# Kernel optimization log

Hardware: AMD Instinct MI355X
Metric: run time of the kernel (lower is better)

The kernel has to match this reference:

```python
import jax, jax.numpy as jnp
import numpy as np

NUM_MOVIES = 100000
MOVIE_FEAT = 128
USER_FEAT = 128
BATCH = 16384
N_NBRS = 50
D0, D1, D2 = 256, 256, 128  # layer_dims


def setup_inputs() -> dict:
    key = jax.random.key(0)
    ks = jax.random.split(key, 16)
    inp = {
        "users": jax.random.normal(ks[0], (BATCH, USER_FEAT), jnp.float32),
        "pos_movies": jax.random.normal(ks[1], (BATCH, MOVIE_FEAT), jnp.float32),
        "neg_movies": jax.random.normal(ks[2], (BATCH, MOVIE_FEAT), jnp.float32),
        "user_ids": jax.random.randint(ks[3], (BATCH,), 0, BATCH),
        "pos_movie_ids": jax.random.randint(ks[4], (BATCH,), 0, NUM_MOVIES),
        "neg_movie_ids": jax.random.randint(ks[5], (BATCH,), 0, NUM_MOVIES),
        "nbr_ids": jax.random.randint(ks[6], (BATCH, N_NBRS), 0, NUM_MOVIES),
        # learned params / buffers
        "movie_table": jax.random.normal(ks[7], (NUM_MOVIES, MOVIE_FEAT), jnp.float32),
        "Wu": jax.random.normal(ks[8], (USER_FEAT, D0), jnp.float32) * (1.0 / np.sqrt(USER_FEAT)),
        "bu": jnp.zeros((D0,), jnp.float32),
        "Wm": jax.random.normal(ks[9], (MOVIE_FEAT, D0), jnp.float32) * (1.0 / np.sqrt(MOVIE_FEAT)),
        "bm": jnp.zeros((D0,), jnp.float32),
        "W1": jax.random.normal(ks[10], (D0, D1), jnp.float32) * (1.0 / np.sqrt(D0)),
        "b1": jnp.zeros((D1,), jnp.float32),
        "W2": jax.random.normal(ks[11], (D1, D2), jnp.float32) * (1.0 / np.sqrt(D1)),
        "b2": jnp.zeros((D2,), jnp.float32),
    }
    return inp


def reference(users, pos_movies, neg_movies, user_ids, pos_movie_ids, neg_movie_ids,
              nbr_ids, movie_table, Wu, bu, Wm, bm, W1, b1, W2, b2):
    # user_projection / movie_projection
    user_emb = users @ Wu + bu                      # [B, D0]
    movie_emb = movie_table @ Wm + bm               # [N, D0]
    pos_emb = movie_emb[pos_movie_ids]              # [B, D0]
    neg_emb = movie_emb[neg_movie_ids]              # [B, D0]
    # vectorized replacement of the per-user neighbor gather + mean loop
    nbr_mean = jnp.mean(movie_emb[nbr_ids], axis=1)  # [B, N_NBRS, D0] -> [B, D0]
    user_emb = user_emb + nbr_mean
    x = jnp.stack([user_emb, pos_emb, neg_emb], axis=0)  # [3, B, D0]
    x = jax.nn.relu(x @ W1 + b1)
    x = jax.nn.relu(x @ W2 + b2)
    return (x[0], x[1], x[2])
```

## Files before the change

kernel.cpp:

```cpp
#include <hip/hip_runtime.h>
#include <hip/hip_bf16.h>

#define BATCH_N   16384
#define FEAT      128
#define NNBR      50
#define NUM_MOVIES_N 100000

typedef short  short8  __attribute__((ext_vector_type(8)));
typedef float  floatx4 __attribute__((ext_vector_type(4)));

__device__ __forceinline__ __hip_bfloat16 f2bf(float x) { return __float2bfloat16(x); }

__device__ __forceinline__ int sw_idx(int r, int c) {
  return (r << 8) + ((((c >> 3) ^ (r & 7)) << 3) | (c & 7));
}

__global__ __launch_bounds__(256) void conv_table(
    const float* __restrict__ t, __hip_bfloat16* __restrict__ tb) {
  size_t i = ((size_t)blockIdx.x * 256 + threadIdx.x) * 8;
  float4 v0 = *(const float4*)(t + i);
  float4 v1 = *(const float4*)(t + i + 4);
  __hip_bfloat16 o[8];
  o[0] = f2bf(v0.x); o[1] = f2bf(v0.y); o[2] = f2bf(v0.z); o[3] = f2bf(v0.w);
  o[4] = f2bf(v1.x); o[5] = f2bf(v1.y); o[6] = f2bf(v1.z); o[7] = f2bf(v1.w);
  *(short8*)(tb + i) = *(short8*)o;
}

__global__ __launch_bounds__(256) void prep_kernel(
    const float* __restrict__ Wu, const float* __restrict__ Wm,
    const float* __restrict__ W1, const float* __restrict__ W2,
    const float* __restrict__ bu, const float* __restrict__ bm,
    __hip_bfloat16* __restrict__ WcatT, __hip_bfloat16* __restrict__ WmT,
    __hip_bfloat16* __restrict__ W1T,  __hip_bfloat16* __restrict__ W2T,
    float* __restrict__ bc) {
  int idx = blockIdx.x * 256 + threadIdx.x;
  int n = idx & 255, k = idx >> 8;
  float v = (k < 128) ? Wu[k * 256 + n] : Wm[(k - 128) * 256 + n];
  WcatT[n * 256 + k] = f2bf(v);
  W1T[n * 256 + k]   = f2bf(W1[k * 256 + n]);
  if (k < 128) WmT[n * 128 + k] = f2bf(Wm[k * 256 + n]);
  if (idx < 32768) {
    int k2 = idx >> 7, n2 = idx & 127;
    W2T[n2 * 256 + k2] = f2bf(W2[k2 * 128 + n2]);
  }
  if (idx < 256) bc[idx] = bu[idx] + bm[idx];
}

__global__ __launch_bounds__(256) void gather_user(
    const float* __restrict__ users, const int* __restrict__ nbr_ids,
    const __hip_bfloat16* __restrict__ tb, __hip_bfloat16* __restrict__ A_user) {
  int row  = (blockIdx.x << 2) + (threadIdx.x >> 6);
  int lane = threadIdx.x & 63;
  const int* nb = nbr_ids + row * NNBR;
  float ax = 0.f, ay = 0.f;
  #pragma unroll 5
  for (int j = 0; j < NNBR; ++j) {
    int id = nb[j];
    __hip_bfloat162 v = ((const __hip_bfloat162*)(tb + (size_t)id * FEAT))[lane];
    ax += __bfloat162float(v.x); ay += __bfloat162float(v.y);
  }
  ax *= (1.f / NNBR); ay *= (1.f / NNBR);
  float2 uv = ((const float2*)(users + (size_t)row * FEAT))[lane];
  __hip_bfloat162* dst = (__hip_bfloat162*)(A_user + (size_t)row * (2 * FEAT));
  __hip_bfloat162 t0; t0.x = f2bf(uv.x); t0.y = f2bf(uv.y);
  __hip_bfloat162 t1; t1.x = f2bf(ax);   t1.y = f2bf(ay);
  dst[lane]      = t0;
  dst[64 + lane] = t1;
}

__global__ __launch_bounds__(256, 2) void fused_mlp(
    const __hip_bfloat16* __restrict__ A_user,
    const __hip_bfloat16* __restrict__ tb,
    const int* __restrict__ pos_ids, const int* __restrict__ neg_ids,
    const __hip_bfloat16* __restrict__ WcatT,
    const __hip_bfloat16* __restrict__ WmT,
    const __hip_bfloat16* __restrict__ W1T,
    const __hip_bfloat16* __restrict__ W2T,
    const float* __restrict__ bc, const float* __restrict__ bmv,
    const float* __restrict__ b1, const float* __restrict__ b2,
    float* __restrict__ out) {
  __shared__ __hip_bfloat16 A_lds[64 * 256];
  __shared__ __hip_bfloat16 E_lds[64 * 256];

  const int t    = threadIdx.x;
  const int lane = t & 63, wid = t >> 6;
  const int wm   = wid & 1, wn = wid >> 1;
  const int quad = lane >> 4, lrow = lane & 15;
  const int s    = blockIdx.y;
  const int m0   = blockIdx.x * 64;

  if (s == 0) {
    #pragma unroll
    for (int c = 0; c < 8; ++c) {
      int ch = t + c * 256;
      int r = ch >> 5, kc = (ch & 31) << 3;
      *(short8*)&A_lds[sw_idx(r, kc)] =
          *(const short8*)(A_user + ((size_t)(m0 + r) << 8) + kc);
    }
  } else {
    const int* ids = (s == 1) ? pos_ids : neg_ids;
    #pragma unroll
    for (int c = 0; c < 4; ++c) {
      int ch = t + c * 256;
      int r = ch >> 4, kc = (ch & 15) << 3;
      int id = ids[m0 + r];
      *(short8*)&A_lds[sw_idx(r, kc)] =
          *(const short8*)(tb + ((size_t)id << 7) + kc);
    }
  }
  __syncthreads();

  const __hip_bfloat16* W0 = (s == 0) ? WcatT : WmT;
  const float* bias0 = (s == 0) ? bc : bmv;
  const int K0 = (s == 0) ? 256 : 128;

  {
    floatx4 acc[2][8] = {};
    for (int k0 = 0; k0 < K0; k0 += 32) {
      short8 af[2];
      #pragma unroll
      for (int i = 0; i < 2; ++i)
        af[i] = *(const short8*)&A_lds[sw_idx(wm * 32 + i * 16 + lrow, k0 + quad * 8)];
      #pragma unroll
      for (int j = 0; j < 8; ++j) {
        int n = wn * 128 + j * 16 + lrow;
        short8 bf = *(const short8*)(W0 + (size_t)n * K0 + k0 + quad * 8);
        #pragma unroll
        for (int i = 0; i < 2; ++i)
          acc[i][j] = __builtin_amdgcn_mfma_f32_16x16x32_bf16(af[i], bf, acc[i][j], 0, 0, 0);
      }
    }
    #pragma unroll
    for (int j = 0; j < 8; ++j) {
      int col = wn * 128 + j * 16 + lrow;
      float bv = bias0[col];
      #pragma unroll
      for (int i = 0; i < 2; ++i)
        #pragma unroll
        for (int r = 0; r < 4; ++r) {
          int row = wm * 32 + i * 16 + quad * 4 + r;
          E_lds[sw_idx(row, col)] = f2bf(acc[i][j][r] + bv);
        }
    }
  }
  __syncthreads();

  {
    floatx4 acc[2][8] = {};
    for (int k0 = 0; k0 < 256; k0 += 32) {
      short8 af[2];
      #pragma unroll
      for (int i = 0; i < 2; ++i)
        af[i] = *(const short8*)&E_lds[sw_idx(wm * 32 + i * 16 + lrow, k0 + quad * 8)];
      #pragma unroll
      for (int j = 0; j < 8; ++j) {
        int n = wn * 128 + j * 16 + lrow;
        short8 bf = *(const short8*)(W1T + ((size_t)n << 8) + k0 + quad * 8);
        #pragma unroll
        for (int i = 0; i < 2; ++i)
          acc[i][j] = __builtin_amdgcn_mfma_f32_16x16x32_bf16(af[i], bf, acc[i][j], 0, 0, 0);
      }
    }
    #pragma unroll
    for (int j = 0; j < 8; ++j) {
      int col = wn * 128 + j * 16 + lrow;
      float bv = b1[col];
      #pragma unroll
      for (int i = 0; i < 2; ++i)
        #pragma unroll
        for (int r = 0; r < 4; ++r) {
          int row = wm * 32 + i * 16 + quad * 4 + r;
          A_lds[sw_idx(row, col)] = f2bf(fmaxf(acc[i][j][r] + bv, 0.f));
        }
    }
  }
  __syncthreads();

  {
    floatx4 acc[2][4] = {};
    for (int k0 = 0; k0 < 256; k0 += 32) {
      short8 af[2];
      #pragma unroll
      for (int i = 0; i < 2; ++i)
        af[i] = *(const short8*)&A_lds[sw_idx(wm * 32 + i * 16 + lrow, k0 + quad * 8)];
      #pragma unroll
      for (int j = 0; j < 4; ++j) {
        int n = wn * 64 + j * 16 + lrow;
        short8 bf = *(const short8*)(W2T + ((size_t)n << 8) + k0 + quad * 8);
        #pragma unroll
        for (int i = 0; i < 2; ++i)
          acc[i][j] = __builtin_amdgcn_mfma_f32_16x16x32_bf16(af[i], bf, acc[i][j], 0, 0, 0);
      }
    }
    #pragma unroll
    for (int j = 0; j < 4; ++j) {
      int col = wn * 64 + j * 16 + lrow;
      float bv = b2[col];
      #pragma unroll
      for (int i = 0; i < 2; ++i)
        #pragma unroll
        for (int r = 0; r < 4; ++r) {
          int row = wm * 32 + i * 16 + quad * 4 + r;
          float v = fmaxf(acc[i][j][r] + bv, 0.f);
          out[((size_t)s * BATCH_N + m0 + row) * 128 + col] = v;
        }
    }
  }
}

extern "C" void kernel_launch(void* const* d_in, const int* in_sizes, int n_in,
                              void* d_out, int out_size, void* d_ws, size_t ws_size,
                              hipStream_t stream) {
  const float* users   = (const float*)d_in[0];
  const int*   pos_ids = (const int*)d_in[4];
  const int*   neg_ids = (const int*)d_in[5];
  const int*   nbr_ids = (const int*)d_in[6];
  const float* table   = (const float*)d_in[7];
  const float* Wu = (const float*)d_in[8];
  const float* bu = (const float*)d_in[9];
  const float* Wm = (const float*)d_in[10];
  const float* bm = (const float*)d_in[11];
  const float* W1 = (const float*)d_in[12];
  const float* b1 = (const float*)d_in[13];
  const float* W2 = (const float*)d_in[14];
  const float* b2 = (const float*)d_in[15];
  float* out = (float*)d_out;

  char* p = (char*)d_ws;
  auto carve = [&](size_t bytes) { char* r = p; p += (bytes + 255) & ~(size_t)255; return r; };
  __hip_bfloat16* tb     = (__hip_bfloat16*)carve((size_t)NUM_MOVIES_N * FEAT * 2);
  __hip_bfloat16* WcatT  = (__hip_bfloat16*)carve(256 * 256 * 2);
  __hip_bfloat16* WmT    = (__hip_bfloat16*)carve(256 * 128 * 2);
  __hip_bfloat16* W1T    = (__hip_bfloat16*)carve(256 * 256 * 2);
  __hip_bfloat16* W2T    = (__hip_bfloat16*)carve(128 * 256 * 2);
  float*          bc     = (float*)carve(256 * 4);
  __hip_bfloat16* A_user = (__hip_bfloat16*)carve((size_t)BATCH_N * 256 * 2);

  conv_table<<<NUM_MOVIES_N * FEAT / (256 * 8), 256, 0, stream>>>(table, tb);
  prep_kernel<<<256, 256, 0, stream>>>(Wu, Wm, W1, W2, bu, bm,
                                       WcatT, WmT, W1T, W2T, bc);
  gather_user<<<BATCH_N / 4, 256, 0, stream>>>(users, nbr_ids, tb, A_user);
  fused_mlp<<<dim3(BATCH_N / 64, 3), 256, 0, stream>>>(
      A_user, tb, pos_ids, neg_ids, WcatT, WmT, W1T, W2T,
      bc, bm, b1, b2, out);
}
```

Before: 219.1 us.

## Stage weights through LDS via global_load_lds and widen neighbor gather loads

The fused MLP now stages each 32-wide K slice of the weight matrix into LDS with direct global-to-LDS loads, using a swizzled layout, instead of having every wave read B fragments from global memory. Input tiles are also loaded with global_load_lds. The three streams are interleaved along a 1D grid so blocks that share an m-tile run close together. The neighbor gather now uses 16-byte loads with four neighbors in flight per wave, combined by a cross-lane shuffle reduction. The cost is two barriers per K step, and the layers are reused with in-place LDS buffers (E_lds doubles as weight staging), so correctness depends on the barrier ordering.

Measured after the change: 214.9 us. No clear change (-1.9%).

```diff
diff --git a/kernel.cpp b/kernel.cpp
--- a/kernel.cpp
+++ b/kernel.cpp
@@ -8,11 +8,21 @@
 
 typedef short  short8  __attribute__((ext_vector_type(8)));
 typedef float  floatx4 __attribute__((ext_vector_type(4)));
+typedef unsigned int u32;
 
 __device__ __forceinline__ __hip_bfloat16 f2bf(float x) { return __float2bfloat16(x); }
-
-__device__ __forceinline__ int sw_idx(int r, int c) {
-  return (r << 8) + ((((c >> 3) ^ (r & 7)) << 3) | (c & 7));
+__device__ __forceinline__ float bfb2f(short s) {
+  union { u32 u; float f; } c; c.u = ((u32)(unsigned short)s) << 16; return c.f;
+}
+
+__device__ __forceinline__ void gld16(const __hip_bfloat16* g, __hip_bfloat16* l) {
+  __builtin_amdgcn_global_load_lds(
+      (const __attribute__((address_space(1))) u32*)g,
+      (__attribute__((address_space(3))) u32*)l, 16, 0, 0);
+}
+
+__device__ __forceinline__ floatx4 mfma16(short8 a, short8 b, floatx4 c) {
+  return __builtin_amdgcn_mfma_f32_16x16x32_bf16(a, b, c, 0, 0, 0);
 }
 
 __global__ __launch_bounds__(256) void conv_table(
@@ -51,21 +61,88 @@
     const __hip_bfloat16* __restrict__ tb, __hip_bfloat16* __restrict__ A_user) {
   int row  = (blockIdx.x << 2) + (threadIdx.x >> 6);
   int lane = threadIdx.x & 63;
+  int quad = lane >> 4, sl = lane & 15;
   const int* nb = nbr_ids + row * NNBR;
-  float ax = 0.f, ay = 0.f;
-  #pragma unroll 5
-  for (int j = 0; j < NNBR; ++j) {
-    int id = nb[j];
-    __hip_bfloat162 v = ((const __hip_bfloat162*)(tb + (size_t)id * FEAT))[lane];
-    ax += __bfloat162float(v.x); ay += __bfloat162float(v.y);
-  }
-  ax *= (1.f / NNBR); ay *= (1.f / NNBR);
+  float acc[8] = {0.f, 0.f, 0.f, 0.f, 0.f, 0.f, 0.f, 0.f};
+  #pragma unroll
+  for (int it = 0; it < 13; ++it) {
+    int j = it * 4 + quad;
+    if (j < NNBR) {
+      int id = nb[j];
+      short8 v = *(const short8*)(tb + (size_t)id * FEAT + sl * 8);
+      #pragma unroll
+      for (int e = 0; e < 8; ++e) acc[e] += bfb2f(v[e]);
+    }
+  }
+  __hip_bfloat16 o[8];
+  #pragma unroll
+  for (int e = 0; e < 8; ++e) {
+    float v = acc[e];
+    v += __shfl_xor(v, 16, 64);
+    v += __shfl_xor(v, 32, 64);
+    o[e] = f2bf(v * (1.f / NNBR));
+  }
+  if (quad == 0)
+    *(short8*)(A_user + (size_t)row * 256 + 128 + sl * 8) = *(short8*)o;
   float2 uv = ((const float2*)(users + (size_t)row * FEAT))[lane];
-  __hip_bfloat162* dst = (__hip_bfloat162*)(A_user + (size_t)row * (2 * FEAT));
   __hip_bfloat162 t0; t0.x = f2bf(uv.x); t0.y = f2bf(uv.y);
-  __hip_bfloat162 t1; t1.x = f2bf(ax);   t1.y = f2bf(ay);
-  dst[lane]      = t0;
-  dst[64 + lane] = t1;
+  ((__hip_bfloat162*)(A_user + (size_t)row * 256))[lane] = t0;
+}
+
+template <int K0, int NCOL, bool RELU, bool TOGLB>
+__device__ __forceinline__ void run_layer(
+    const __hip_bfloat16* Ain, __hip_bfloat16* Bst,
+    const __hip_bfloat16* __restrict__ W, const float* __restrict__ bias,
+    __hip_bfloat16* Olds, float* __restrict__ Oglb,
+    int t, int wm, int wn, int quad, int lrow, long m0) {
+  constexpr int KK = K0 / 32;
+  constexpr int JN = NCOL / 32;
+  floatx4 acc[2][JN] = {};
+  for (int kc = 0; kc < KK; ++kc) {
+    const int k0 = kc * 32;
+    __syncthreads();
+    #pragma unroll
+    for (int i = 0; i < NCOL / 64; ++i) {
+      int c = t + i * 256;
+      int n = c >> 2, q = c & 3;
+      gld16(W + (size_t)n * K0 + k0 + ((q ^ ((n >> 1) & 3)) << 3),
+            Bst + (c << 3));
+    }
+    __syncthreads();
+    short8 af[2];
+    #pragma unroll
+    for (int i = 0; i < 2; ++i) {
+      int r = wm * 32 + i * 16 + lrow;
+      af[i] = *(const short8*)&Ain[r * K0 + ((((k0 >> 3) + quad) ^ (r & 7)) << 3)];
+    }
+    #pragma unroll
+    for (int j = 0; j < JN; ++j) {
+      int n = wn * (NCOL / 2) + j * 16 + lrow;
+      short8 bf = *(const short8*)&Bst[n * 32 + ((quad ^ ((n >> 1) & 3)) << 3)];
+      acc[0][j] = mfma16(af[0], bf, acc[0][j]);
+      acc[1][j] = mfma16(af[1], bf, acc[1][j]);
+    }
+  }
+  __syncthreads();
+  #pragma unroll
+  for (int j = 0; j < JN; ++j) {
+    int col = wn * (NCOL / 2) + j * 16 + lrow;
+    float bv = bias[col];
+    #pragma unroll
+    for (int i = 0; i < 2; ++i)
+      #pragma unroll
+      for (int r = 0; r < 4; ++r) {
+        int row = wm * 32 + i * 16 + quad * 4 + r;
+        float v = acc[i][j][r] + bv;
+        if (RELU) v = fmaxf(v, 0.f);
+        if (TOGLB) {
+          Oglb[(m0 + row) * 128 + col] = v;
+        } else {
+          int ch = col >> 3;
+          Olds[row * 256 + (((ch ^ (row & 7)) << 3) | (col & 7))] = f2bf(v);
+        }
+      }
+  }
 }
 
 __global__ __launch_bounds__(256, 2) void fused_mlp(
@@ -86,126 +163,43 @@
   const int lane = t & 63, wid = t >> 6;
   const int wm   = wid & 1, wn = wid >> 1;
   const int quad = lane >> 4, lrow = lane & 15;
-  const int s    = blockIdx.y;
-  const int m0   = blockIdx.x * 64;
+  const int bx   = blockIdx.x;
+  const int s    = bx % 3;
+  const long m0  = (long)(bx / 3) * 64;
 
   if (s == 0) {
     #pragma unroll
-    for (int c = 0; c < 8; ++c) {
-      int ch = t + c * 256;
-      int r = ch >> 5, kc = (ch & 31) << 3;
-      *(short8*)&A_lds[sw_idx(r, kc)] =
-          *(const short8*)(A_user + ((size_t)(m0 + r) << 8) + kc);
+    for (int i = 0; i < 8; ++i) {
+      int c = t + i * 256;
+      int r = c >> 5, kq = c & 31;
+      gld16(A_user + ((size_t)(m0 + r) << 8) + ((kq ^ (r & 7)) << 3),
+            A_lds + (c << 3));
     }
   } else {
     const int* ids = (s == 1) ? pos_ids : neg_ids;
     #pragma unroll
-    for (int c = 0; c < 4; ++c) {
-      int ch = t + c * 256;
-      int r = ch >> 4, kc = (ch & 15) << 3;
+    for (int i = 0; i < 4; ++i) {
+      int c = t + i * 256;
+      int r = c >> 4, kq = c & 15;
       int id = ids[m0 + r];
-      *(short8*)&A_lds[sw_idx(r, kc)] =
-          *(const short8*)(tb + ((size_t)id << 7) + kc);
-    }
-  }
-  __syncthreads();
-
-  const __hip_bfloat16* W0 = (s == 0) ? WcatT : WmT;
-  const float* bias0 = (s == 0) ? bc : bmv;
-  const int K0 = (s == 0) ? 256 : 128;
-
-  {
-    floatx4 acc[2][8] = {};
-    for (int k0 = 0; k0 < K0; k0 += 32) {
-      short8 af[2];
-      #pragma unroll
-      for (int i = 0; i < 2; ++i)
-        af[i] = *(const short8*)&A_lds[sw_idx(wm * 32 + i * 16 + lrow, k0 + quad * 8)];
-      #pragma unroll
-      for (int j = 0; j < 8; ++j) {
-        int n = wn * 128 + j * 16 + lrow;
-        short8 bf = *(const short8*)(W0 + (size_t)n * K0 + k0 + quad * 8);
-        #pragma unroll
-        for (int i = 0; i < 2; ++i)
-          acc[i][j] = __builtin_amdgcn_mfma_f32_16x16x32_bf16(af[i], bf, acc[i][j], 0, 0, 0);
-      }
-    }
-    #pragma unroll
-    for (int j = 0; j < 8; ++j) {
-      int col = wn * 128 + j * 16 + lrow;
-      float bv = bias0[col];
-      #pragma unroll
-      for (int i = 0; i < 2; ++i)
-        #pragma unroll
-        for (int r = 0; r < 4; ++r) {
-          int row = wm * 32 + i * 16 + quad * 4 + r;
-          E_lds[sw_idx(row, col)] = f2bf(acc[i][j][r] + bv);
-        }
-    }
-  }
-  __syncthreads();
-
-  {
-    floatx4 acc[2][8] = {};
-    for (int k0 = 0; k0 < 256; k0 += 32) {
-      short8 af[2];
-      #pragma unroll
-      for (int i = 0; i < 2; ++i)
-        af[i] = *(const short8*)&E_lds[sw_idx(wm * 32 + i * 16 + lrow, k0 + quad * 8)];
-      #pragma unroll
-      for (int j = 0; j < 8; ++j) {
-        int n = wn * 128 + j * 16 + lrow;
-        short8 bf = *(const short8*)(W1T + ((size_t)n << 8) + k0 + quad * 8);
-        #pragma unroll
-        for (int i = 0; i < 2; ++i)
-          acc[i][j] = __builtin_amdgcn_mfma_f32_16x16x32_bf16(af[i], bf, acc[i][j], 0, 0, 0);
-      }
-    }
-    #pragma unroll
-    for (int j = 0; j < 8; ++j) {
-      int col = wn * 128 + j * 16 + lrow;
-      float bv = b1[col];
-      #pragma unroll
-      for (int i = 0; i < 2; ++i)
-        #pragma unroll
-        for (int r = 0; r < 4; ++r) {
-          int row = wm * 32 + i * 16 + quad * 4 + r;
-          A_lds[sw_idx(row, col)] = f2bf(fmaxf(acc[i][j][r] + bv, 0.f));
-        }
-    }
-  }
-  __syncthreads();
-
-  {
-    floatx4 acc[2][4] = {};
-    for (int k0 = 0; k0 < 256; k0 += 32) {
-      short8 af[2];
-      #pragma unroll
-      for (int i = 0; i < 2; ++i)
-        af[i] = *(const short8*)&A_lds[sw_idx(wm * 32 + i * 16 + lrow, k0 + quad * 8)];
-      #pragma unroll
-      for (int j = 0; j < 4; ++j) {
-        int n = wn * 64 + j * 16 + lrow;
-        short8 bf = *(const short8*)(W2T + ((size_t)n << 8) + k0 + quad * 8);
-        #pragma unroll
-        for (int i = 0; i < 2; ++i)
-          acc[i][j] = __builtin_amdgcn_mfma_f32_16x16x32_bf16(af[i], bf, acc[i][j], 0, 0, 0);
-      }
-    }
-    #pragma unroll
-    for (int j = 0; j < 4; ++j) {
-      int col = wn * 64 + j * 16 + lrow;
-      float bv = b2[col];
-      #pragma unroll
-      for (int i = 0; i < 2; ++i)
-        #pragma unroll
-        for (int r = 0; r < 4; ++r) {
-          int row = wm * 32 + i * 16 + quad * 4 + r;
-          float v = fmaxf(acc[i][j][r] + bv, 0.f);
-          out[((size_t)s * BATCH_N + m0 + row) * 128 + col] = v;
-        }
-    }
-  }
+      gld16(tb + ((size_t)id << 7) + ((kq ^ (r & 7)) << 3),
+            A_lds + (c << 3));
+    }
+  }
+
+  if (s == 0)
+    run_layer<256, 256, false, false>(A_lds, E_lds, WcatT, bc, E_lds, nullptr,
+                                      t, wm, wn, quad, lrow, m0);
+  else
+    run_layer<128, 256, false, false>(A_lds, E_lds, WmT, bmv, E_lds, nullptr,
+                                      t, wm, wn, quad, lrow, m0);
+
+  run_layer<256, 256, true, false>(E_lds, A_lds, W1T, b1, A_lds, nullptr,
+                                   t, wm, wn, quad, lrow, m0);
+
+  run_layer<256, 128, true, true>(A_lds, E_lds, W2T, b2, nullptr,
+                                  out + (size_t)s * BATCH_N * 128,
+                                  t, wm, wn, quad, lrow, m0);
 }
 
 extern "C" void kernel_launch(void* const* d_in, const int* in_sizes, int n_in,
@@ -240,7 +234,7 @@
   prep_kernel<<<256, 256, 0, stream>>>(Wu, Wm, W1, W2, bu, bm,
                                        WcatT, WmT, W1T, W2T, bc);
   gather_user<<<BATCH_N / 4, 256, 0, stream>>>(users, nbr_ids, tb, A_user);
-  fused_mlp<<<dim3(BATCH_N / 64, 3), 256, 0, stream>>>(
+  fused_mlp<<<dim3(3 * BATCH_N / 64), 256, 0, stream>>>(
       A_user, tb, pos_ids, neg_ids, WcatT, WmT, W1T, W2T,
       bc, bm, b1, b2, out);
 }
```
